# Kernel tuning notes

Measured on AMD Instinct MI355X. Metric: run time of the kernel, lower is better.

The kernel has to match this reference:

```python
import jax, jax.numpy as jnp
import numpy as np

NEG_INF = -1e30


def setup_inputs() -> dict:
    key = jax.random.key(0)
    k1, k2, k3, k4, k5, k6 = jax.random.split(key, 6)
    T, B = 256, 8
    Din, Dm, A = 256, 256, 128
    input = jax.random.normal(k1, (T, B, Din), dtype=jnp.float32)
    memory = jax.random.normal(k2, (T, B, Dm), dtype=jnp.float32)
    memory_mask = jax.random.randint(k3, (T, B), 0, 2, dtype=jnp.int32)
    # first Linear weight [A, Din+Dm] split into input / memory halves (additive decomposition)
    scale1 = 1.0 / np.sqrt(Din + Dm)
    Wi = jax.random.uniform(k4, (Din, A), minval=-scale1, maxval=scale1, dtype=jnp.float32)
    Wm = jax.random.uniform(k5, (Dm, A), minval=-scale1, maxval=scale1, dtype=jnp.float32)
    # second Linear weight [1, A] -> vector [A]
    scale2 = 1.0 / np.sqrt(A)
    v = jax.random.uniform(k6, (A,), minval=-scale2, maxval=scale2, dtype=jnp.float32)
    return {"input": input, "memory": memory, "memory_mask": memory_mask,
            "Wi": Wi, "Wm": Wm, "v": v}


def reference(input, memory, memory_mask, Wi, Wm, v):
    # input: [T, B, Din], memory: [T, B, Dm], memory_mask: [T, B]
    # Additive (Bahdanau) scores: v . tanh(Wi x_s + Wm m_t). Concat+Linear on
    # [x; m] with block weight [Wi; Wm] equals the sum of the two projections.
    ip = jnp.einsum('tbd,da->tba', input, Wi)[:, None]    # [T, 1, B, A]
    mp = jnp.einsum('tbd,da->tba', memory, Wm)[None]      # [1, T, B, A]
    logits = jnp.einsum('stba,a->stb', jnp.tanh(ip + mp), v)  # [T, T, B]
    masked = jnp.where(memory_mask[None] != 0, logits, NEG_INF)
    score = jax.nn.softmax(masked, axis=1)                # softmax over key dim
    # NOTE: original module weights `input` (not memory) as values.
    context = jnp.einsum('stb,tbd->sbd', score, input)    # [T, B, Din]
    return jnp.concatenate([context, input], axis=-1)      # [T, B, 2*Din]
```

## Files before the change

### kernel.cpp

```cpp
#include <hip/hip_runtime.h>

#define T_DIM 256
#define B_DIM 8
#define DIN   256
#define DM    256
#define A_DIM 128
#define AP_DIM (A_DIM / 2)
#define NEG_INF_F (-1e30f)
#define PRESCALE 2.885390081777927f
#define PROJ_TT 8
#define S_TILE  4

__global__ __launch_bounds__(512) void proj_kernel(
    const float* __restrict__ input, const float* __restrict__ memory,
    const float* __restrict__ Wi, const float* __restrict__ Wm,
    float* __restrict__ EIP, float* __restrict__ EM2)
{
    __shared__ float xin[PROJ_TT][DIN];
    __shared__ float xmem[PROJ_TT][DM];
    const int row0 = blockIdx.x * PROJ_TT;
    const int tid  = threadIdx.x;

    for (int i = tid; i < PROJ_TT * DIN; i += 512) {
        const int r = i >> 8, d = i & 255;
        xin[r][d]  = input[(row0 + r) * DIN + d];
        xmem[r][d] = memory[(row0 + r) * DM + d];
    }
    __syncthreads();

    const int group = tid >> 7;
    const int a     = tid & 127;
    const int r0    = (group & 1) * 4;

    if (group < 2) {
        float acc[4] = {0.f, 0.f, 0.f, 0.f};
        #pragma unroll 8
        for (int d = 0; d < DIN; ++d) {
            const float w = Wi[d * A_DIM + a];
            #pragma unroll
            for (int r = 0; r < 4; ++r)
                acc[r] = fmaf(xin[r0 + r][d], w, acc[r]);
        }
        #pragma unroll
        for (int r = 0; r < 4; ++r)
            EIP[(row0 + r0 + r) * A_DIM + a] =
                __builtin_amdgcn_exp2f(acc[r] * PRESCALE);
    } else {
        float acc[4] = {0.f, 0.f, 0.f, 0.f};
        #pragma unroll 8
        for (int d = 0; d < DM; ++d) {
            const float w = Wm[d * A_DIM + a];
            #pragma unroll
            for (int r = 0; r < 4; ++r)
                acc[r] = fmaf(xmem[r0 + r][d], w, acc[r]);
        }
        #pragma unroll
        for (int r = 0; r < 4; ++r) {
            const int row = row0 + r0 + r;
            const int t = row / B_DIM, b = row % B_DIM;
            EM2[(((size_t)b * AP_DIM + (a >> 1)) * T_DIM + t) * 2 + (a & 1)] =
                __builtin_amdgcn_exp2f(acc[r] * PRESCALE);
        }
    }
}

__device__ inline float warp_red_max(float v) {
    #pragma unroll
    for (int o = 32; o > 0; o >>= 1) v = fmaxf(v, __shfl_xor(v, o, 64));
    return v;
}
__device__ inline float warp_red_sum(float v) {
    #pragma unroll
    for (int o = 32; o > 0; o >>= 1) v += __shfl_xor(v, o, 64);
    return v;
}

__global__ __launch_bounds__(256) void attn_kernel(
    const float* __restrict__ input, const int* __restrict__ mask,
    const float* __restrict__ v, const float* __restrict__ EIP,
    const float* __restrict__ EM2, float* __restrict__ out)
{
    __shared__ float4 eipv[2][AP_DIM];
    __shared__ float4 v4[AP_DIM];
    __shared__ float sc[S_TILE][T_DIM];
    __shared__ float redm[S_TILE][4];
    __shared__ float4 part[4][S_TILE][64];

    const int blk = blockIdx.x;
    const int b   = blk % B_DIM;
    const int s0  = (blk / B_DIM) * S_TILE;
    const int tid = threadIdx.x;
    const int lane = tid & 63;
    const int wave = tid >> 6;

    {
        float* eipf = (float*)eipv;
        float* v4f  = (float*)v4;
        if (tid < A_DIM) {
            const int a = tid, ap = a >> 1, j = a & 1;
            #pragma unroll
            for (int sp = 0; sp < 2; ++sp) {
                eipf[(sp * AP_DIM + ap) * 4 + j]     = EIP[((s0 + 2 * sp + 0) * B_DIM + b) * A_DIM + a];
                eipf[(sp * AP_DIM + ap) * 4 + 2 + j] = EIP[((s0 + 2 * sp + 1) * B_DIM + b) * A_DIM + a];
            }
            v4f[ap * 4 + j] = v[a];
        }
        if (tid < AP_DIM) {
            v4f[tid * 4 + 2] = v[2 * tid] + v[2 * tid + 1];
            v4f[tid * 4 + 3] = 0.f;
        }
    }
    __syncthreads();

    const int t = tid;
    float acc[S_TILE] = {0.f, 0.f, 0.f, 0.f};
    const float2* em_p = (const float2*)EM2 + (size_t)b * AP_DIM * T_DIM + t;
    #pragma unroll 4
    for (int ap = 0; ap < AP_DIM; ++ap) {
        const float2 em = em_p[(size_t)ap * T_DIM];
        const float4 vv = v4[ap];
        #pragma unroll
        for (int sp = 0; sp < 2; ++sp) {
            const float4 ei = eipv[sp][ap];
            float ea  = ei.x * em.x;
            float eb  = ei.y * em.y;
            float den = fmaf(ea, eb, (ea + eb) + 1.f);
            float num = fmaf(vv.x, eb, fmaf(vv.y, ea, vv.z));
            acc[2 * sp + 0] = fmaf(num, __builtin_amdgcn_rcpf(den), acc[2 * sp + 0]);
            ea  = ei.z * em.x;
            eb  = ei.w * em.y;
            den = fmaf(ea, eb, (ea + eb) + 1.f);
            num = fmaf(vv.x, eb, fmaf(vv.y, ea, vv.z));
            acc[2 * sp + 1] = fmaf(num, __builtin_amdgcn_rcpf(den), acc[2 * sp + 1]);
        }
    }

    const bool valid = (mask[t * B_DIM + b] != 0);
    float l[S_TILE], ex[S_TILE], su[S_TILE];
    #pragma unroll
    for (int s = 0; s < S_TILE; ++s)
        l[s] = valid ? (-2.f * acc[s]) : NEG_INF_F;

    #pragma unroll
    for (int s = 0; s < S_TILE; ++s) {
        const float m = warp_red_max(l[s]);
        if (lane == 0) redm[s][wave] = m;
    }
    __syncthreads();
    #pragma unroll
    for (int s = 0; s < S_TILE; ++s) {
        const float m = fmaxf(fmaxf(redm[s][0], redm[s][1]), fmaxf(redm[s][2], redm[s][3]));
        ex[s] = __expf(l[s] - m);
        su[s] = warp_red_sum(ex[s]);
    }
    __syncthreads();
    if (lane == 0) {
        #pragma unroll
        for (int s = 0; s < S_TILE; ++s) redm[s][wave] = su[s];
    }
    __syncthreads();
    #pragma unroll
    for (int s = 0; s < S_TILE; ++s) {
        const float sum = (redm[s][0] + redm[s][1]) + (redm[s][2] + redm[s][3]);
        sc[s][t] = ex[s] * __builtin_amdgcn_rcpf(sum);
    }
    __syncthreads();

    const int d4 = lane;
    const int tq = wave;
    float4 c[S_TILE];
    #pragma unroll
    for (int s = 0; s < S_TILE; ++s) c[s] = {0.f, 0.f, 0.f, 0.f};
    const float4* in_b4 = (const float4*)(input + b * DIN) + d4;
    const int t_base = tq * 64;
    #pragma unroll 4
    for (int i = 0; i < 64; ++i) {
        const int t2 = t_base + i;
        const float4 xv = in_b4[(size_t)t2 * (B_DIM * DIN / 4)];
        #pragma unroll
        for (int s = 0; s < S_TILE; ++s) {
            const float sv = sc[s][t2];
            c[s].x = fmaf(sv, xv.x, c[s].x);
            c[s].y = fmaf(sv, xv.y, c[s].y);
            c[s].z = fmaf(sv, xv.z, c[s].z);
            c[s].w = fmaf(sv, xv.w, c[s].w);
        }
    }
    #pragma unroll
    for (int s = 0; s < S_TILE; ++s) part[tq][s][d4] = c[s];
    __syncthreads();

    {
        const int s = wave;
        const float4 p0 = part[0][s][d4];
        const float4 p1 = part[1][s][d4];
        const float4 p2 = part[2][s][d4];
        const float4 p3 = part[3][s][d4];
        float4 cc;
        cc.x = (p0.x + p1.x) + (p2.x + p3.x);
        cc.y = (p0.y + p1.y) + (p2.y + p3.y);
        cc.z = (p0.z + p1.z) + (p2.z + p3.z);
        cc.w = (p0.w + p1.w) + (p2.w + p3.w);
        const int row = (s0 + s) * B_DIM + b;
        *((float4*)(out + (size_t)row * (2 * DIN)) + d4) = cc;
        const float4 inrow = *((const float4*)(input + (size_t)row * DIN) + d4);
        *((float4*)(out + (size_t)row * (2 * DIN) + DIN) + d4) = inrow;
    }
}

extern "C" void kernel_launch(void* const* d_in, const int* in_sizes, int n_in,
                              void* d_out, int out_size, void* d_ws, size_t ws_size,
                              hipStream_t stream) {
    const float* input  = (const float*)d_in[0];
    const float* memory = (const float*)d_in[1];
    const int*   mask   = (const int*)d_in[2];
    const float* Wi     = (const float*)d_in[3];
    const float* Wm     = (const float*)d_in[4];
    const float* v      = (const float*)d_in[5];
    float* out = (float*)d_out;

    float* EIP = (float*)d_ws;
    float* EM2 = EIP + (size_t)T_DIM * B_DIM * A_DIM;

    proj_kernel<<<(T_DIM * B_DIM) / PROJ_TT, 512, 0, stream>>>(input, memory, Wi, Wm, EIP, EM2);
    attn_kernel<<<(T_DIM / S_TILE) * B_DIM, 256, 0, stream>>>(input, mask, v, EIP, EM2, out);
}
```

Before: 97.55 us.

## Read projection rows directly from global memory and move input copy into proj kernel

The projection kernel no longer stages input and memory rows in shared memory and drops the block barrier. Each thread group instead reads its four rows straight from global memory, which are wave-uniform broadcast loads likely served by cache. The copy of input into the second half of the output now happens in the projection kernel instead of the attention kernel, taking that store off the attention kernel's tail. The risk is more global load instructions in the inner FMA loop in place of LDS reads.

```diff
diff --git a/kernel.cpp b/kernel.cpp
--- a/kernel.cpp
+++ b/kernel.cpp
@@ -14,46 +14,34 @@
 __global__ __launch_bounds__(512) void proj_kernel(
     const float* __restrict__ input, const float* __restrict__ memory,
     const float* __restrict__ Wi, const float* __restrict__ Wm,
-    float* __restrict__ EIP, float* __restrict__ EM2)
+    float* __restrict__ EIP, float* __restrict__ EM2,
+    float* __restrict__ out)
 {
-    __shared__ float xin[PROJ_TT][DIN];
-    __shared__ float xmem[PROJ_TT][DM];
     const int row0 = blockIdx.x * PROJ_TT;
     const int tid  = threadIdx.x;
-
-    for (int i = tid; i < PROJ_TT * DIN; i += 512) {
-        const int r = i >> 8, d = i & 255;
-        xin[r][d]  = input[(row0 + r) * DIN + d];
-        xmem[r][d] = memory[(row0 + r) * DM + d];
-    }
-    __syncthreads();
-
     const int group = tid >> 7;
     const int a     = tid & 127;
     const int r0    = (group & 1) * 4;
 
+    const float* __restrict__ X = (group < 2) ? input : memory;
+    const float* __restrict__ W = (group < 2) ? Wi : Wm;
+    const float* __restrict__ xr = X + (size_t)(row0 + r0) * DIN;
+
+    float acc[4] = {0.f, 0.f, 0.f, 0.f};
+    #pragma unroll 8
+    for (int d = 0; d < DIN; ++d) {
+        const float w = W[d * A_DIM + a];
+        #pragma unroll
+        for (int r = 0; r < 4; ++r)
+            acc[r] = fmaf(xr[r * DIN + d], w, acc[r]);
+    }
+
     if (group < 2) {
-        float acc[4] = {0.f, 0.f, 0.f, 0.f};
-        #pragma unroll 8
-        for (int d = 0; d < DIN; ++d) {
-            const float w = Wi[d * A_DIM + a];
-            #pragma unroll
-            for (int r = 0; r < 4; ++r)
-                acc[r] = fmaf(xin[r0 + r][d], w, acc[r]);
-        }
         #pragma unroll
         for (int r = 0; r < 4; ++r)
             EIP[(row0 + r0 + r) * A_DIM + a] =
                 __builtin_amdgcn_exp2f(acc[r] * PRESCALE);
     } else {
-        float acc[4] = {0.f, 0.f, 0.f, 0.f};
-        #pragma unroll 8
-        for (int d = 0; d < DM; ++d) {
-            const float w = Wm[d * A_DIM + a];
-            #pragma unroll
-            for (int r = 0; r < 4; ++r)
-                acc[r] = fmaf(xmem[r0 + r][d], w, acc[r]);
-        }
         #pragma unroll
         for (int r = 0; r < 4; ++r) {
             const int row = row0 + r0 + r;
@@ -61,6 +49,14 @@
             EM2[(((size_t)b * AP_DIM + (a >> 1)) * T_DIM + t) * 2 + (a & 1)] =
                 __builtin_amdgcn_exp2f(acc[r] * PRESCALE);
         }
+    }
+
+    {
+        const int r  = tid >> 6;
+        const int d4 = tid & 63;
+        const int row = row0 + r;
+        const float4 xv = *((const float4*)(input + (size_t)row * DIN) + d4);
+        *((float4*)(out + (size_t)row * (2 * DIN) + DIN) + d4) = xv;
     }
 }
 
@@ -203,8 +199,6 @@
         cc.w = (p0.w + p1.w) + (p2.w + p3.w);
         const int row = (s0 + s) * B_DIM + b;
         *((float4*)(out + (size_t)row * (2 * DIN)) + d4) = cc;
-        const float4 inrow = *((const float4*)(input + (size_t)row * DIN) + d4);
-        *((float4*)(out + (size_t)row * (2 * DIN) + DIN) + d4) = inrow;
     }
 }
 
@@ -222,6 +216,6 @@
     float* EIP = (float*)d_ws;
     float* EM2 = EIP + (size_t)T_DIM * B_DIM * A_DIM;
 
-    proj_kernel<<<(T_DIM * B_DIM) / PROJ_TT, 512, 0, stream>>>(input, memory, Wi, Wm, EIP, EM2);
+    proj_kernel<<<(T_DIM * B_DIM) / PROJ_TT, 512, 0, stream>>>(input, memory, Wi, Wm, EIP, EM2, out);
     attn_kernel<<<(T_DIM / S_TILE) * B_DIM, 256, 0, stream>>>(input, mask, v, EIP, EM2, out);
 }
```

Measured after the change: 107.9 us. +10.6%, slower.
